# Kernel tuning notes

Hardware: AMD Instinct MI355X
Metric: run time of the kernel (lower is better)

Reference implementation:

```python
import jax, jax.numpy as jnp
import numpy as np

NUM_USER = 200000
NUM_ITEM = 100000
DIM = 64
NUM_LAYER = 2  # hardcoded in LightGCN.__init__ (lgn_single(..., num_layer=2))
AVG_DEG = 16
N = NUM_USER + NUM_ITEM
E = N * AVG_DEG
BATCH = 16384


def setup_inputs() -> dict:
    key = jax.random.key(0)
    k = jax.random.split(key, 8)
    emb_user = jax.random.normal(k[0], (NUM_USER, DIM), jnp.float32) * 0.05
    emb_item = jax.random.normal(k[1], (NUM_ITEM, DIM), jnp.float32) * 0.05
    # COO sparse normalized adjacency: out[row] += vals * x[col]
    graph_row = jax.random.randint(k[2], (E,), 0, N, dtype=jnp.int32)
    graph_col = jax.random.randint(k[3], (E,), 0, N, dtype=jnp.int32)
    graph_vals = jax.random.uniform(k[4], (E,), jnp.float32) / AVG_DEG
    user_nodes = jax.random.randint(k[5], (BATCH,), 0, NUM_USER, dtype=jnp.int32)
    pos_item_nodes = jax.random.randint(k[6], (BATCH,), 0, NUM_ITEM, dtype=jnp.int32) + NUM_USER
    neg_item_nodes = jax.random.randint(k[7], (BATCH,), 0, NUM_ITEM, dtype=jnp.int32) + NUM_USER
    return {
        "emb_user": emb_user,
        "emb_item": emb_item,
        "graph_vals": graph_vals,
        "graph_row": graph_row,
        "graph_col": graph_col,
        "user_nodes": user_nodes,
        "pos_item_nodes": pos_item_nodes,
        "neg_item_nodes": neg_item_nodes,
    }


def _spmm(vals, row, col, x):
    # torch.sparse.mm(graph, x) with graph in COO form
    return jax.ops.segment_sum(vals[:, None] * x[col], row, num_segments=N)


def reference(emb_user, emb_item, graph_vals, graph_row, graph_col,
              user_nodes, pos_item_nodes, neg_item_nodes):
    # LGN_single.forward: concat, propagate, mean over layer stack
    all_emb = jnp.concatenate([emb_user, emb_item], axis=0)  # [N, D]
    acc = all_emb
    e = all_emb
    for _ in range(NUM_LAYER):
        e = _spmm(graph_vals, graph_row, graph_col, e)
        acc = acc + e
    light_out = acc / (NUM_LAYER + 1)  # mean of stacked embeddings
    # LightGCN.forward: gather + elementwise dot scores
    u = light_out[user_nodes]          # [B, D]
    p = light_out[pos_item_nodes]      # [B, D]
    n = light_out[neg_item_nodes]      # [B, D]
    pos_scores = jnp.sum(u * p, axis=1)
    neg_scores = jnp.sum(u * n, axis=1)
    return jnp.stack([pos_scores, neg_scores])  # [2, B]
```

## Files before the change

kernel.cpp:

```cpp
#include <hip/hip_runtime.h>

#define DIM 64
#define CHUNK 8192
#define MAXNB 512
#define BSHIFT 10
#define RPB 1024
#define PADMASK 7

__device__ __forceinline__ unsigned short f2bf(float f) {
    unsigned int u = __float_as_uint(f);
    return (unsigned short)((u + 0x7FFFu + ((u >> 16) & 1u)) >> 16);
}
__device__ __forceinline__ float4 bf2f4(unsigned int lo, unsigned int hi) {
    float4 x;
    x.x = __uint_as_float(lo << 16);
    x.y = __uint_as_float(lo & 0xffff0000u);
    x.z = __uint_as_float(hi << 16);
    x.w = __uint_as_float(hi & 0xffff0000u);
    return x;
}
__device__ __forceinline__ float4 bf2f4(uint2 g) { return bf2f4(g.x, g.y); }

__device__ __forceinline__ int blockScan256(int v, int* sh) {
    int t = threadIdx.x;
    sh[t] = v;
    __syncthreads();
    for (int off = 1; off < 256; off <<= 1) {
        int x = (t >= off) ? sh[t - off] : 0;
        __syncthreads();
        sh[t] += x;
        __syncthreads();
    }
    return sh[t];
}


__global__ void conv2_k(const float* __restrict__ u, const float* __restrict__ it,
                        int nu, int ntot, unsigned short* __restrict__ o) {
    int i = blockIdx.x * blockDim.x + threadIdx.x;
    int stride = gridDim.x * blockDim.x;
    int n8 = ntot >> 3;
    for (int t = i; t < n8; t += stride) {
        int e = t * 8;
        const float* src = (e < nu) ? (u + e) : (it + (e - nu));
        float4 x = *(const float4*)src;
        float4 y = *(const float4*)(src + 4);
        uint4 v;
        v.x = (unsigned)f2bf(x.x) | ((unsigned)f2bf(x.y) << 16);
        v.y = (unsigned)f2bf(x.z) | ((unsigned)f2bf(x.w) << 16);
        v.z = (unsigned)f2bf(y.x) | ((unsigned)f2bf(y.y) << 16);
        v.w = (unsigned)f2bf(y.z) | ((unsigned)f2bf(y.w) << 16);
        ((uint4*)o)[t] = v;
    }
}


__global__ void p1a_hist(const int* __restrict__ row, int E, int NB,
                         int* __restrict__ counts) {
    __shared__ int h[MAXNB];
    for (int b = threadIdx.x; b < NB; b += 256) h[b] = 0;
    __syncthreads();
    int base = blockIdx.x * CHUNK;
    int end = min(base + CHUNK, E);
    int vend = base + ((end - base) & ~3);
    for (int i = base + threadIdx.x * 4; i < vend; i += 1024) {
        int4 r = *(const int4*)(row + i);
        atomicAdd(&h[r.x >> BSHIFT], 1);
        atomicAdd(&h[r.y >> BSHIFT], 1);
        atomicAdd(&h[r.z >> BSHIFT], 1);
        atomicAdd(&h[r.w >> BSHIFT], 1);
    }
    for (int i = vend + threadIdx.x; i < end; i += 256) atomicAdd(&h[row[i] >> BSHIFT], 1);
    __syncthreads();
    int blk = blockIdx.x;
    for (int b = threadIdx.x; b < NB; b += 256) counts[(size_t)blk * NB + b] = h[b];
}

__global__ void p1b_scan(int* __restrict__ counts, int NBLK, int NB,
                         int* __restrict__ bucketTotal) {
    int b = blockIdx.x, t = threadIdx.x;
    __shared__ int sh[256];
    int v[8];
    int run = 0;
#pragma unroll
    for (int i = 0; i < 8; i++) {
        int idx = t * 8 + i;
        int c = (idx < NBLK) ? counts[(size_t)idx * NB + b] : 0;
        v[i] = run;
        run += c;
    }
    int inc = blockScan256(run, sh);
    int excl = inc - run;
#pragma unroll
    for (int i = 0; i < 8; i++) {
        int idx = t * 8 + i;
        if (idx < NBLK) counts[(size_t)idx * NB + b] = v[i] + excl;
    }
    if (t == 255) bucketTotal[b] = sh[255];
}

__global__ void p_scan_tot(const int* __restrict__ bucketTotal, int NB,
                           int* __restrict__ bucketStart) {
    int t = threadIdx.x;
    __shared__ int sh[256];
    int v[8];
    int run = 0;
#pragma unroll
    for (int i = 0; i < 8; i++) {
        int idx = t * 8 + i;
        int c = (idx < NB) ? bucketTotal[idx] : 0;
        v[i] = run;
        run += c;
    }
    int inc = blockScan256(run, sh);
    int excl = inc - run;
#pragma unroll
    for (int i = 0; i < 8; i++) {
        int idx = t * 8 + i;
        if (idx < NB) bucketStart[idx] = v[i] + excl;
    }
    if (t == 255) bucketStart[NB] = sh[255];
}

__global__ void p1c_scatter(const int* __restrict__ row, const int* __restrict__ col,
                            const float* __restrict__ vals, int E, int NB,
                            const int* __restrict__ counts, const int* __restrict__ bucketStart,
                            int2* __restrict__ bdata) {
    __shared__ int cur[MAXNB];
    int blk = blockIdx.x;
    for (int b = threadIdx.x; b < NB; b += 256)
        cur[b] = bucketStart[b] + counts[(size_t)blk * NB + b];
    __syncthreads();
    int base = blk * CHUNK;
    int end = min(base + CHUNK, E);
    int vend = base + ((end - base) & ~3);
    for (int i = base + threadIdx.x * 4; i < vend; i += 1024) {
        int4 r = *(const int4*)(row + i);
        int4 c = *(const int4*)(col + i);
        float4 v = *(const float4*)(vals + i);
        int p0 = atomicAdd(&cur[r.x >> BSHIFT], 1);
        int p1 = atomicAdd(&cur[r.y >> BSHIFT], 1);
        int p2 = atomicAdd(&cur[r.z >> BSHIFT], 1);
        int p3 = atomicAdd(&cur[r.w >> BSHIFT], 1);
        bdata[p0] = make_int2(((r.x & (RPB - 1)) << 20) | c.x, __float_as_int(v.x));
        bdata[p1] = make_int2(((r.y & (RPB - 1)) << 20) | c.y, __float_as_int(v.y));
        bdata[p2] = make_int2(((r.z & (RPB - 1)) << 20) | c.z, __float_as_int(v.z));
        bdata[p3] = make_int2(((r.w & (RPB - 1)) << 20) | c.w, __float_as_int(v.w));
    }
    for (int i = vend + threadIdx.x; i < end; i += 256) {
        int r = row[i];
        int p = atomicAdd(&cur[r >> BSHIFT], 1);
        bdata[p] = make_int2(((r & (RPB - 1)) << 20) | col[i], __float_as_int(vals[i]));
    }
}

__global__ void p2_group(const int2* __restrict__ bdata, const int* __restrict__ bucketStart,
                         int NB, int N, int padSlop,
                         int* __restrict__ rowStart, int* __restrict__ rowLen,
                         int2* __restrict__ pairs) {
    __shared__ int hist[RPB];
    __shared__ int sh[256];
    __shared__ int cur[RPB];
    int b = blockIdx.x, t = threadIdx.x;
    int s0 = bucketStart[b], s1 = bucketStart[b + 1];
    int pbase = s0 + b * padSlop;
    for (int i = t; i < RPB; i += 256) hist[i] = 0;
    __syncthreads();
    for (int i = s0 + t; i < s1; i += 256)
        atomicAdd(&hist[(bdata[i].x >> 20) & (RPB - 1)], 1);
    __syncthreads();
    int v[4];
    int run = 0;
#pragma unroll
    for (int i = 0; i < 4; i++) {
        int h = hist[t * 4 + i];
        int hp = (h + PADMASK) & ~PADMASK;
        v[i] = run;
        run += hp;
    }
    int inc = blockScan256(run, sh);
    int excl = inc - run;
#pragma unroll
    for (int i = 0; i < 4; i++) {
        int r = (b << BSHIFT) + t * 4 + i;
        int st = excl + v[i];
        if (r < N) {
            int h = hist[t * 4 + i];
            rowStart[r] = pbase + st;
            rowLen[r] = (h + PADMASK) & ~PADMASK;
        }
        cur[t * 4 + i] = st;
    }
    __syncthreads();
    for (int i = s0 + t; i < s1; i += 256) {
        int2 e = bdata[i];
        int rl = (e.x >> 20) & (RPB - 1);
        int pos = atomicAdd(&cur[rl], 1);
        pairs[pbase + pos] = make_int2((e.x & 0xFFFFF) << 7, e.y);
    }
    __syncthreads();
#pragma unroll
    for (int i = 0; i < 4; i++) {
        int h = hist[t * 4 + i];
        int hp = (h + PADMASK) & ~PADMASK;
        int st = excl + v[i];
        for (int p = st + h; p < st + hp; p++)
            pairs[pbase + p] = make_int2(0, 0);
    }
}


__global__ void spmm1_k(const unsigned short* __restrict__ emb16,
                        const int* __restrict__ rowStart, const int* __restrict__ rowLen,
                        const int2* __restrict__ pairs,
                        int n_total, unsigned short* __restrict__ e1) {
    int wave = (blockIdx.x * blockDim.x + threadIdx.x) >> 6;
    int lane = threadIdx.x & 63;
    if (wave >= n_total) return;
    int eg = lane >> 3, dp = lane & 7;
    unsigned off0 = dp * 16u;
    const char* base = (const char*)emb16;
    int len = rowLen[wave];
    const int2* pp = pairs + rowStart[wave];
    float4 aA0 = {0.f, 0.f, 0.f, 0.f}, aA1 = {0.f, 0.f, 0.f, 0.f};
    float4 aB0 = {0.f, 0.f, 0.f, 0.f}, aB1 = {0.f, 0.f, 0.f, 0.f};
    int k = 0;
    for (; k + 16 <= len; k += 16) {
        int4 q = *(const int4*)(pp + k + 2 * eg);
        uint4 g0 = *(const uint4*)(base + ((unsigned)q.x + off0));
        uint4 g1 = *(const uint4*)(base + ((unsigned)q.z + off0));
        float v0 = __int_as_float(q.y), v1 = __int_as_float(q.w);
        float4 x0 = bf2f4(g0.x, g0.y), x1 = bf2f4(g0.z, g0.w);
        float4 y0 = bf2f4(g1.x, g1.y), y1 = bf2f4(g1.z, g1.w);
        aA0.x += v0 * x0.x; aA0.y += v0 * x0.y; aA0.z += v0 * x0.z; aA0.w += v0 * x0.w;
        aA1.x += v0 * x1.x; aA1.y += v0 * x1.y; aA1.z += v0 * x1.z; aA1.w += v0 * x1.w;
        aB0.x += v1 * y0.x; aB0.y += v1 * y0.y; aB0.z += v1 * y0.z; aB0.w += v1 * y0.w;
        aB1.x += v1 * y1.x; aB1.y += v1 * y1.y; aB1.z += v1 * y1.z; aB1.w += v1 * y1.w;
    }
    if (k < len) {
        int2 p = pp[k + eg];
        uint4 g0 = *(const uint4*)(base + ((unsigned)p.x + off0));
        float v0 = __int_as_float(p.y);
        float4 x0 = bf2f4(g0.x, g0.y), x1 = bf2f4(g0.z, g0.w);
        aA0.x += v0 * x0.x; aA0.y += v0 * x0.y; aA0.z += v0 * x0.z; aA0.w += v0 * x0.w;
        aA1.x += v0 * x1.x; aA1.y += v0 * x1.y; aA1.z += v0 * x1.z; aA1.w += v0 * x1.w;
    }
    float4 s0, s1;
    s0.x = aA0.x + aB0.x; s0.y = aA0.y + aB0.y; s0.z = aA0.z + aB0.z; s0.w = aA0.w + aB0.w;
    s1.x = aA1.x + aB1.x; s1.y = aA1.y + aB1.y; s1.z = aA1.z + aB1.z; s1.w = aA1.w + aB1.w;
#pragma unroll
    for (int m = 8; m <= 32; m <<= 1) {
        s0.x += __shfl_xor(s0.x, m); s0.y += __shfl_xor(s0.y, m);
        s0.z += __shfl_xor(s0.z, m); s0.w += __shfl_xor(s0.w, m);
        s1.x += __shfl_xor(s1.x, m); s1.y += __shfl_xor(s1.y, m);
        s1.z += __shfl_xor(s1.z, m); s1.w += __shfl_xor(s1.w, m);
    }
    if (eg == 0) {
        uint4 o;
        o.x = (unsigned)f2bf(s0.x) | ((unsigned)f2bf(s0.y) << 16);
        o.y = (unsigned)f2bf(s0.z) | ((unsigned)f2bf(s0.w) << 16);
        o.z = (unsigned)f2bf(s1.x) | ((unsigned)f2bf(s1.y) << 16);
        o.w = (unsigned)f2bf(s1.z) | ((unsigned)f2bf(s1.w) << 16);
        *(uint4*)(e1 + (size_t)wave * DIM + dp * 8) = o;
    }
}


__global__ void final_k(const float* __restrict__ emb_user, const float* __restrict__ emb_item,
                        int n_user, const unsigned short* __restrict__ e1,
                        const int* __restrict__ rowStart, const int* __restrict__ rowLen,
                        const int2* __restrict__ pairs,
                        const int* __restrict__ u_nodes, const int* __restrict__ p_nodes,
                        const int* __restrict__ n_nodes, int B, float* __restrict__ out) {
    int wave = (blockIdx.x * blockDim.x + threadIdx.x) >> 6;
    int lane = threadIdx.x & 63;
    if (wave >= B) return;
    int eg = lane >> 4, dp = lane & 15;
    unsigned off0 = dp * 8u;
    const char* base = (const char*)e1;
    int nid[3] = {u_nodes[wave], p_nodes[wave], n_nodes[wave]};
    float4 l[3];
#pragma unroll
    for (int j = 0; j < 3; j++) {
        int r = nid[j];
        const float* base0 = (r < n_user) ? (emb_user + (size_t)r * DIM)
                                          : (emb_item + (size_t)(r - n_user) * DIM);
        float4 acc = *(const float4*)(base0 + dp * 4);
        float4 t1 = bf2f4(*(const uint2*)(e1 + (size_t)r * DIM + dp * 4));
        acc.x += t1.x; acc.y += t1.y; acc.z += t1.z; acc.w += t1.w;
        int len = rowLen[r];
        const int2* pp = pairs + rowStart[r];
        float4 a0 = {0.f, 0.f, 0.f, 0.f}, a1 = {0.f, 0.f, 0.f, 0.f};
        float4 a2 = {0.f, 0.f, 0.f, 0.f}, a3 = {0.f, 0.f, 0.f, 0.f};
        int k = 0;
        for (; k + 16 <= len; k += 16) {
            int4 q0 = *(const int4*)(pp + k + 2 * eg);
            int4 q1 = *(const int4*)(pp + k + 8 + 2 * eg);
            uint2 g0 = *(const uint2*)(base + ((unsigned)q0.x + off0));
            uint2 g1 = *(const uint2*)(base + ((unsigned)q0.z + off0));
            uint2 g2 = *(const uint2*)(base + ((unsigned)q1.x + off0));
            uint2 g3 = *(const uint2*)(base + ((unsigned)q1.z + off0));
            float v0 = __int_as_float(q0.y), v1 = __int_as_float(q0.w);
            float v2 = __int_as_float(q1.y), v3 = __int_as_float(q1.w);
            float4 x0 = bf2f4(g0), x1 = bf2f4(g1), x2 = bf2f4(g2), x3 = bf2f4(g3);
            a0.x += v0 * x0.x; a0.y += v0 * x0.y; a0.z += v0 * x0.z; a0.w += v0 * x0.w;
            a1.x += v1 * x1.x; a1.y += v1 * x1.y; a1.z += v1 * x1.z; a1.w += v1 * x1.w;
            a2.x += v2 * x2.x; a2.y += v2 * x2.y; a2.z += v2 * x2.z; a2.w += v2 * x2.w;
            a3.x += v3 * x3.x; a3.y += v3 * x3.y; a3.z += v3 * x3.z; a3.w += v3 * x3.w;
        }
        for (; k < len; k += 8) {
            int4 q0 = *(const int4*)(pp + k + 2 * eg);
            uint2 g0 = *(const uint2*)(base + ((unsigned)q0.x + off0));
            uint2 g1 = *(const uint2*)(base + ((unsigned)q0.z + off0));
            float v0 = __int_as_float(q0.y), v1 = __int_as_float(q0.w);
            float4 x0 = bf2f4(g0), x1 = bf2f4(g1);
            a0.x += v0 * x0.x; a0.y += v0 * x0.y; a0.z += v0 * x0.z; a0.w += v0 * x0.w;
            a1.x += v1 * x1.x; a1.y += v1 * x1.y; a1.z += v1 * x1.z; a1.w += v1 * x1.w;
        }
        float4 s;
        s.x = (a0.x + a1.x) + (a2.x + a3.x);
        s.y = (a0.y + a1.y) + (a2.y + a3.y);
        s.z = (a0.z + a1.z) + (a2.z + a3.z);
        s.w = (a0.w + a1.w) + (a2.w + a3.w);
        s.x += __shfl_xor(s.x, 16); s.y += __shfl_xor(s.y, 16);
        s.z += __shfl_xor(s.z, 16); s.w += __shfl_xor(s.w, 16);
        s.x += __shfl_xor(s.x, 32); s.y += __shfl_xor(s.y, 32);
        s.z += __shfl_xor(s.z, 32); s.w += __shfl_xor(s.w, 32);
        l[j].x = (acc.x + s.x) * (1.0f / 3.0f);
        l[j].y = (acc.y + s.y) * (1.0f / 3.0f);
        l[j].z = (acc.z + s.z) * (1.0f / 3.0f);
        l[j].w = (acc.w + s.w) * (1.0f / 3.0f);
    }
    float ps = l[0].x * l[1].x + l[0].y * l[1].y + l[0].z * l[1].z + l[0].w * l[1].w;
    float ns = l[0].x * l[2].x + l[0].y * l[2].y + l[0].z * l[2].z + l[0].w * l[2].w;
    ps += __shfl_xor(ps, 1); ns += __shfl_xor(ns, 1);
    ps += __shfl_xor(ps, 2); ns += __shfl_xor(ns, 2);
    ps += __shfl_xor(ps, 4); ns += __shfl_xor(ns, 4);
    ps += __shfl_xor(ps, 8); ns += __shfl_xor(ns, 8);
    if (lane == 0) {
        out[wave] = ps;
        out[B + wave] = ns;
    }
}

extern "C" void kernel_launch(void* const* d_in, const int* in_sizes, int n_in,
                              void* d_out, int out_size, void* d_ws, size_t ws_size,
                              hipStream_t stream) {
    const float* emb_user = (const float*)d_in[0];
    const float* emb_item = (const float*)d_in[1];
    const float* gvals    = (const float*)d_in[2];
    const int*   grow     = (const int*)d_in[3];
    const int*   gcol     = (const int*)d_in[4];
    const int*   unodes   = (const int*)d_in[5];
    const int*   pnodes   = (const int*)d_in[6];
    const int*   nnodes   = (const int*)d_in[7];
    float* out = (float*)d_out;

    int n_user = in_sizes[0] / DIM;
    int n_item = in_sizes[1] / DIM;
    int N = n_user + n_item;
    int E = in_sizes[2];
    int B = in_sizes[5];
    int NB = (N + RPB - 1) >> BSHIFT;
    int NBLK = (E + CHUNK - 1) / CHUNK;
    int padSlop = RPB * PADMASK;

    char* ws = (char*)d_ws;
    size_t off = 0;
    auto alloc = [&](size_t bytes) -> void* {
        void* p = ws + off;
        off = (off + bytes + 255) & ~(size_t)255;
        return p;
    };
    size_t embBytes = (size_t)N * DIM * 2;
    size_t countsBytes = (size_t)NBLK * NB * 4;
    size_t regionBBytes = (size_t)E * 8 > embBytes ? (size_t)E * 8 : embBytes;
    size_t regionABytes = countsBytes > embBytes ? countsBytes : embBytes;
    size_t pairsBytes = ((size_t)E + (size_t)NB * padSlop) * 8;

    int*  rowStart    = (int*)alloc((size_t)N * 4);
    int*  rowLen      = (int*)alloc((size_t)N * 4);
    int*  bucketTotal = (int*)alloc((size_t)MAXNB * 4);
    int*  bucketStart = (int*)alloc((size_t)(MAXNB + 1) * 4);
    int2* pairs       = (int2*)alloc(pairsBytes);
    char* regionB = (char*)alloc(regionBBytes);
    int2*           bdata = (int2*)regionB;
    unsigned short* emb16 = (unsigned short*)regionB;
    char* regionA = (char*)alloc(regionABytes);
    int*            counts = (int*)regionA;
    unsigned short* e1     = (unsigned short*)regionA;
    (void)n_in; (void)out_size; (void)ws_size;

    p1a_hist<<<NBLK, 256, 0, stream>>>(grow, E, NB, counts);
    p1b_scan<<<NB, 256, 0, stream>>>(counts, NBLK, NB, bucketTotal);
    p_scan_tot<<<1, 256, 0, stream>>>(bucketTotal, NB, bucketStart);
    p1c_scatter<<<NBLK, 256, 0, stream>>>(grow, gcol, gvals, E, NB, counts, bucketStart, bdata);
    p2_group<<<NB, 256, 0, stream>>>(bdata, bucketStart, NB, N, padSlop,
                                     rowStart, rowLen, pairs);

    conv2_k<<<2048, 256, 0, stream>>>(emb_user, emb_item, n_user * DIM, N * DIM, emb16);

    spmm1_k<<<(N + 3) / 4, 256, 0, stream>>>(emb16, rowStart, rowLen, pairs, N, e1);
    final_k<<<(B + 3) / 4, 256, 0, stream>>>(emb_user, emb_item, n_user, e1,
                                             rowStart, rowLen, pairs,
                                             unodes, pnodes, nnodes, B, out);
}
```

Baseline: 305.4 us.

## Fuse embedding bf16 conversion into scatter kernel and halve rows per bucket

Adds extra blocks to the edge-scatter kernel that convert user/item embeddings to bf16 in parallel, when the workspace can hold separate bdata and emb16 buffers. This removes a separate conversion launch and overlaps conversion with the atomic-heavy scatter. It also shrinks buckets from 1024 to 512 rows, doubling bucket count, which gives more p2_group blocks and smaller shared histograms but larger count matrices and more padding slop. Falls back to the old aliased layout when the workspace is too small.

Result: slower. 321.3 us (+5.2%).

```diff
diff --git a/kernel.cpp b/kernel.cpp
--- a/kernel.cpp
+++ b/kernel.cpp
@@ -2,10 +2,11 @@
 
 #define DIM 64
 #define CHUNK 8192
-#define MAXNB 512
-#define BSHIFT 10
-#define RPB 1024
+#define MAXNB 1024
+#define BSHIFT 9
+#define RPB 512
 #define PADMASK 7
+#define CONVB 512
 
 __device__ __forceinline__ unsigned short f2bf(float f) {
     unsigned int u = __float_as_uint(f);
@@ -122,35 +123,57 @@
     if (t == 255) bucketStart[NB] = sh[255];
 }
 
-__global__ void p1c_scatter(const int* __restrict__ row, const int* __restrict__ col,
-                            const float* __restrict__ vals, int E, int NB,
-                            const int* __restrict__ counts, const int* __restrict__ bucketStart,
-                            int2* __restrict__ bdata) {
+__global__ void p1c_conv(const int* __restrict__ row, const int* __restrict__ col,
+                         const float* __restrict__ vals, int E, int NB,
+                         const int* __restrict__ counts, const int* __restrict__ bucketStart,
+                         int2* __restrict__ bdata, int NBLK,
+                         const float* __restrict__ u, const float* __restrict__ it,
+                         int nu, int ntot, unsigned short* __restrict__ o) {
     __shared__ int cur[MAXNB];
     int blk = blockIdx.x;
-    for (int b = threadIdx.x; b < NB; b += 256)
-        cur[b] = bucketStart[b] + counts[(size_t)blk * NB + b];
-    __syncthreads();
-    int base = blk * CHUNK;
-    int end = min(base + CHUNK, E);
-    int vend = base + ((end - base) & ~3);
-    for (int i = base + threadIdx.x * 4; i < vend; i += 1024) {
-        int4 r = *(const int4*)(row + i);
-        int4 c = *(const int4*)(col + i);
-        float4 v = *(const float4*)(vals + i);
-        int p0 = atomicAdd(&cur[r.x >> BSHIFT], 1);
-        int p1 = atomicAdd(&cur[r.y >> BSHIFT], 1);
-        int p2 = atomicAdd(&cur[r.z >> BSHIFT], 1);
-        int p3 = atomicAdd(&cur[r.w >> BSHIFT], 1);
-        bdata[p0] = make_int2(((r.x & (RPB - 1)) << 20) | c.x, __float_as_int(v.x));
-        bdata[p1] = make_int2(((r.y & (RPB - 1)) << 20) | c.y, __float_as_int(v.y));
-        bdata[p2] = make_int2(((r.z & (RPB - 1)) << 20) | c.z, __float_as_int(v.z));
-        bdata[p3] = make_int2(((r.w & (RPB - 1)) << 20) | c.w, __float_as_int(v.w));
-    }
-    for (int i = vend + threadIdx.x; i < end; i += 256) {
-        int r = row[i];
-        int p = atomicAdd(&cur[r >> BSHIFT], 1);
-        bdata[p] = make_int2(((r & (RPB - 1)) << 20) | col[i], __float_as_int(vals[i]));
+    if (blk < NBLK) {
+        for (int b = threadIdx.x; b < NB; b += 256)
+            cur[b] = bucketStart[b] + counts[(size_t)blk * NB + b];
+        __syncthreads();
+        int base = blk * CHUNK;
+        int end = min(base + CHUNK, E);
+        int vend = base + ((end - base) & ~3);
+        for (int i = base + threadIdx.x * 4; i < vend; i += 1024) {
+            int4 r = *(const int4*)(row + i);
+            int4 c = *(const int4*)(col + i);
+            float4 v = *(const float4*)(vals + i);
+            int p0 = atomicAdd(&cur[r.x >> BSHIFT], 1);
+            int p1 = atomicAdd(&cur[r.y >> BSHIFT], 1);
+            int p2 = atomicAdd(&cur[r.z >> BSHIFT], 1);
+            int p3 = atomicAdd(&cur[r.w >> BSHIFT], 1);
+            bdata[p0] = make_int2(((r.x & (RPB - 1)) << 20) | c.x, __float_as_int(v.x));
+            bdata[p1] = make_int2(((r.y & (RPB - 1)) << 20) | c.y, __float_as_int(v.y));
+            bdata[p2] = make_int2(((r.z & (RPB - 1)) << 20) | c.z, __float_as_int(v.z));
+            bdata[p3] = make_int2(((r.w & (RPB - 1)) << 20) | c.w, __float_as_int(v.w));
+        }
+        for (int i = vend + threadIdx.x; i < end; i += 256) {
+            int r = row[i];
+            int p = atomicAdd(&cur[r >> BSHIFT], 1);
+            bdata[p] = make_int2(((r & (RPB - 1)) << 20) | col[i], __float_as_int(vals[i]));
+        }
+    } else {
+        int cb = blk - NBLK;
+        int nConv = gridDim.x - NBLK;
+        int i = cb * 256 + threadIdx.x;
+        int stride = nConv * 256;
+        int n8 = ntot >> 3;
+        for (int t = i; t < n8; t += stride) {
+            int e = t * 8;
+            const float* src = (e < nu) ? (u + e) : (it + (e - nu));
+            float4 x = *(const float4*)src;
+            float4 y = *(const float4*)(src + 4);
+            uint4 v;
+            v.x = (unsigned)f2bf(x.x) | ((unsigned)f2bf(x.y) << 16);
+            v.y = (unsigned)f2bf(x.z) | ((unsigned)f2bf(x.w) << 16);
+            v.z = (unsigned)f2bf(y.x) | ((unsigned)f2bf(y.y) << 16);
+            v.w = (unsigned)f2bf(y.z) | ((unsigned)f2bf(y.w) << 16);
+            ((uint4*)o)[t] = v;
+        }
     }
 }
 
@@ -169,11 +192,11 @@
     for (int i = s0 + t; i < s1; i += 256)
         atomicAdd(&hist[(bdata[i].x >> 20) & (RPB - 1)], 1);
     __syncthreads();
-    int v[4];
+    int v[2];
     int run = 0;
 #pragma unroll
-    for (int i = 0; i < 4; i++) {
-        int h = hist[t * 4 + i];
+    for (int i = 0; i < 2; i++) {
+        int h = hist[t * 2 + i];
         int hp = (h + PADMASK) & ~PADMASK;
         v[i] = run;
         run += hp;
@@ -181,15 +204,15 @@
     int inc = blockScan256(run, sh);
     int excl = inc - run;
 #pragma unroll
-    for (int i = 0; i < 4; i++) {
-        int r = (b << BSHIFT) + t * 4 + i;
+    for (int i = 0; i < 2; i++) {
+        int r = (b << BSHIFT) + t * 2 + i;
         int st = excl + v[i];
         if (r < N) {
-            int h = hist[t * 4 + i];
+            int h = hist[t * 2 + i];
             rowStart[r] = pbase + st;
             rowLen[r] = (h + PADMASK) & ~PADMASK;
         }
-        cur[t * 4 + i] = st;
+        cur[t * 2 + i] = st;
     }
     __syncthreads();
     for (int i = s0 + t; i < s1; i += 256) {
@@ -200,8 +223,8 @@
     }
     __syncthreads();
 #pragma unroll
-    for (int i = 0; i < 4; i++) {
-        int h = hist[t * 4 + i];
+    for (int i = 0; i < 2; i++) {
+        int h = hist[t * 2 + i];
         int hp = (h + PADMASK) & ~PADMASK;
         int st = excl + v[i];
         for (int p = st + h; p < st + hp; p++)
@@ -365,6 +388,17 @@
     int NBLK = (E + CHUNK - 1) / CHUNK;
     int padSlop = RPB * PADMASK;
 
+    auto align256 = [](size_t x) { return (x + 255) & ~(size_t)255; };
+    size_t embBytes = (size_t)N * DIM * 2;
+    size_t countsBytes = (size_t)NBLK * NB * 4;
+    size_t bdataBytes = (size_t)E * 8;
+    size_t regionABytes = countsBytes > embBytes ? countsBytes : embBytes;
+    size_t pairsBytes = ((size_t)E + (size_t)NB * padSlop) * 8;
+    size_t fixedBytes = align256((size_t)N * 4) * 2 + align256((size_t)MAXNB * 4) +
+                        align256((size_t)(MAXNB + 1) * 4) + align256(pairsBytes) +
+                        align256(regionABytes);
+    bool sepEmb = fixedBytes + align256(bdataBytes) + align256(embBytes) <= ws_size;
+
     char* ws = (char*)d_ws;
     size_t off = 0;
     auto alloc = [&](size_t bytes) -> void* {
@@ -372,33 +406,37 @@
         off = (off + bytes + 255) & ~(size_t)255;
         return p;
     };
-    size_t embBytes = (size_t)N * DIM * 2;
-    size_t countsBytes = (size_t)NBLK * NB * 4;
-    size_t regionBBytes = (size_t)E * 8 > embBytes ? (size_t)E * 8 : embBytes;
-    size_t regionABytes = countsBytes > embBytes ? countsBytes : embBytes;
-    size_t pairsBytes = ((size_t)E + (size_t)NB * padSlop) * 8;
-
     int*  rowStart    = (int*)alloc((size_t)N * 4);
     int*  rowLen      = (int*)alloc((size_t)N * 4);
     int*  bucketTotal = (int*)alloc((size_t)MAXNB * 4);
     int*  bucketStart = (int*)alloc((size_t)(MAXNB + 1) * 4);
     int2* pairs       = (int2*)alloc(pairsBytes);
-    char* regionB = (char*)alloc(regionBBytes);
-    int2*           bdata = (int2*)regionB;
-    unsigned short* emb16 = (unsigned short*)regionB;
+    int2* bdata;
+    unsigned short* emb16;
+    if (sepEmb) {
+        bdata = (int2*)alloc(bdataBytes);
+        emb16 = (unsigned short*)alloc(embBytes);
+    } else {
+        char* regionB = (char*)alloc(bdataBytes > embBytes ? bdataBytes : embBytes);
+        bdata = (int2*)regionB;
+        emb16 = (unsigned short*)regionB;
+    }
     char* regionA = (char*)alloc(regionABytes);
     int*            counts = (int*)regionA;
     unsigned short* e1     = (unsigned short*)regionA;
-    (void)n_in; (void)out_size; (void)ws_size;
+    (void)n_in; (void)out_size;
 
     p1a_hist<<<NBLK, 256, 0, stream>>>(grow, E, NB, counts);
     p1b_scan<<<NB, 256, 0, stream>>>(counts, NBLK, NB, bucketTotal);
     p_scan_tot<<<1, 256, 0, stream>>>(bucketTotal, NB, bucketStart);
-    p1c_scatter<<<NBLK, 256, 0, stream>>>(grow, gcol, gvals, E, NB, counts, bucketStart, bdata);
+    int nConv = sepEmb ? CONVB : 0;
+    p1c_conv<<<NBLK + nConv, 256, 0, stream>>>(grow, gcol, gvals, E, NB, counts, bucketStart,
+                                               bdata, NBLK,
+                                               emb_user, emb_item, n_user * DIM, N * DIM, emb16);
     p2_group<<<NB, 256, 0, stream>>>(bdata, bucketStart, NB, N, padSlop,
                                      rowStart, rowLen, pairs);
-
-    conv2_k<<<2048, 256, 0, stream>>>(emb_user, emb_item, n_user * DIM, N * DIM, emb16);
+    if (!sepEmb)
+        conv2_k<<<2048, 256, 0, stream>>>(emb_user, emb_item, n_user * DIM, N * DIM, emb16);
 
     spmm1_k<<<(N + 3) / 4, 256, 0, stream>>>(emb16, rowStart, rowLen, pairs, N, e1);
     final_k<<<(B + 3) / 4, 256, 0, stream>>>(emb_user, emb_item, n_user, e1,
```
